# Kernel optimization log

Hardware: AMD Instinct MI355X
Metric: run time of the kernel (lower is better)

## Reference

```python
import jax, jax.numpy as jnp
import numpy as np

B, LQ, H, NH, LK, N = 32, 256, 256, 8, 512, 8192
DH = H // NH
EPS = 1e-12

def layer_norm(x, g, b):
    m = x.mean(-1, keepdims=True)
    v = ((x - m) ** 2).mean(-1, keepdims=True)
    return (x - m) / jnp.sqrt(v + EPS) * g + b

def setup_inputs() -> dict:
    rs = np.random.RandomState(0)
    counts = rs.randint(LK // 2, LK + 1, size=B)  # ragged per-graph edge counts, max = LK
    E = int(counts.sum())
    edge_batch = jnp.asarray(np.repeat(np.arange(B), counts), jnp.int32)
    edge_pos = jnp.asarray(np.concatenate([np.arange(c) for c in counts]), jnp.int32)
    pad_mask = jnp.asarray((np.arange(LK)[None, :] < counts[:, None]).astype(np.float32))
    src = jnp.asarray(rs.randint(0, N, E), jnp.int32)
    dst = jnp.asarray(rs.randint(0, N, E), jnp.int32)
    ks = jax.random.split(jax.random.key(0), 16)
    def rn(i, shape, s=0.02):
        return jax.random.normal(ks[i], shape, jnp.float32) * s
    return dict(
        extended_attention_mask=jnp.zeros((B, 1, 1, LQ), jnp.float32),
        query=rn(0, (B, LQ, H), 1.0),
        rel_embedding_output=rn(1, (E, H), 1.0),
        graph_output=rn(2, (N, H), 1.0),
        src=src, dst=dst, edge_batch=edge_batch, edge_pos=edge_pos, pad_mask=pad_mask,
        Wq=rn(3, (H, H)), bq=jnp.zeros((H,), jnp.float32),
        Wk=rn(4, (2 * H, H)), bk=jnp.zeros((H,), jnp.float32),
        Wv=rn(5, (H, H)), bv=jnp.zeros((H,), jnp.float32),
        Wo=rn(6, (H, H)), bo=jnp.zeros((H,), jnp.float32),
        ln1_g=jnp.ones((H,), jnp.float32), ln1_b=jnp.zeros((H,), jnp.float32),
        W1=rn(7, (H, H)), b1=jnp.zeros((H,), jnp.float32),
        W2=rn(8, (H, H)), b2=jnp.zeros((H,), jnp.float32),
        ln2_g=jnp.ones((H,), jnp.float32), ln2_b=jnp.zeros((H,), jnp.float32),
    )

def reference(extended_attention_mask, query, rel_embedding_output, graph_output,
              src, dst, edge_batch, edge_pos, pad_mask,
              Wq, bq, Wk, bk, Wv, bv, Wo, bo, ln1_g, ln1_b,
              W1, b1, W2, b2, ln2_g, ln2_b):
    # --- memory_transform: edge gather + ragged pad (vectorized scatter) ---
    key_flat = jnp.concatenate([graph_output[src], rel_embedding_output], -1)  # [E, 2H]
    dst_flat = graph_output[dst]                                               # [E, H]
    key_pad = jnp.zeros((B, LK, 2 * H), key_flat.dtype).at[edge_batch, edge_pos].set(key_flat)
    val_pad = jnp.zeros((B, LK, H), dst_flat.dtype).at[edge_batch, edge_pos].set(dst_flat)
    cross_mask = (1.0 - pad_mask)[:, None, None, :] * -10000.0                 # [B,1,1,LK]
    # --- BidiAttention ---
    Q = (query @ Wq + bq).reshape(B, LQ, NH, DH)
    K = (key_pad @ Wk + bk).reshape(B, LK, NH, DH)
    V = (val_pad @ Wv + bv).reshape(B, LK, NH, DH)
    scores = jnp.einsum('bqhd,bkhd->bhqk', Q, K) / np.float32(np.sqrt(DH))
    pq = jax.nn.softmax(scores + cross_mask, axis=-1)
    query_ctx = jnp.einsum('bhqk,bkhd->bqhd', pq, V).reshape(B, LQ, H)
    pv = jax.nn.softmax(scores.transpose(0, 1, 3, 2) + extended_attention_mask, axis=-1)
    value_ctx = jnp.einsum('bhkq,bqhd->bkhd', pv, Q).reshape(B, LK, H)
    # --- RelAwareCross output / gate ---
    query_out = layer_norm(query_ctx @ Wo + bo + query, ln1_g, ln1_b)
    theta = jax.nn.sigmoid(value_ctx @ W1 + b1 + val_pad @ W2 + b2)
    value_new = layer_norm(theta * value_ctx + (1.0 - theta) * val_pad, ln2_g, ln2_b)
    # --- memory_update: unpad + scatter-mean by dst, replace rows with incoming edges ---
    val_edges = value_new[edge_batch, edge_pos]                                # [E, H]
    sums = jax.ops.segment_sum(val_edges, dst, num_segments=N)
    cnts = jax.ops.segment_sum(jnp.ones((val_edges.shape[0],), val_edges.dtype), dst, num_segments=N)
    mean = sums / jnp.maximum(cnts, 1.0)[:, None]
    graph_new = jnp.where((cnts > 0)[:, None], mean, graph_output)
    return (graph_new, query_out)
```

## Files before the change

### kernel.cpp

```cpp
#include <hip/hip_runtime.h>
#include <hip/hip_bf16.h>
#include <string.h>

#define B_ 32
#define LQ_ 256
#define H_ 256
#define NH_ 8
#define LK_ 512
#define N_ 8192
#define DH_ 32

typedef float floatx4 __attribute__((ext_vector_type(4)));
typedef short shortx8 __attribute__((ext_vector_type(8)));

__device__ __forceinline__ short f2b(float f) {
    __hip_bfloat16 h = __float2bfloat16(f);
    short s;
    __builtin_memcpy(&s, &h, 2);
    return s;
}
__device__ __forceinline__ float b2f(short s) {
    unsigned u = ((unsigned)(unsigned short)s) << 16;
    float f;
    __builtin_memcpy(&f, &u, 4);
    return f;
}

__global__ __launch_bounds__(256) void phase1(
    const float* __restrict__ graph, const float* __restrict__ rel,
    const int* __restrict__ src, const int* __restrict__ dst,
    const int* __restrict__ eb, const float* __restrict__ pad_mask,
    const float* __restrict__ Wq, const float* __restrict__ Wk,
    const float* __restrict__ Wv, const float* __restrict__ Wo,
    const float* __restrict__ W1, const float* __restrict__ W2,
    short* __restrict__ WT, short* __restrict__ key_pad,
    short* __restrict__ val_pad, float* __restrict__ zbase, int E) {
    const int bid = blockIdx.x, tid = threadIdx.x;
    if (bid < 8192) {
        int row = bid * 2 + (tid >> 7);
        int t = tid & 127;
        int b = row >> 9, p = row & 511;
        bool valid = pad_mask[row] > 0.5f;
        size_t krow = (size_t)row * 512;
        size_t vrow = (size_t)row * 256;
        int kc = t * 4, vc = t * 2;
        if (valid) {
            int lo = 0, hi = E;
            while (lo < hi) { int mid = (lo + hi) >> 1; if (eb[mid] < b) lo = mid + 1; else hi = mid; }
            int e = lo + p;
            int s = src[e], d = dst[e];
            const float* sp = (kc < 256) ? (graph + (size_t)s * 256 + kc)
                                         : (rel + (size_t)e * 256 + (kc - 256));
            float4 k4 = *(const float4*)sp;
            key_pad[krow + kc + 0] = f2b(k4.x);
            key_pad[krow + kc + 1] = f2b(k4.y);
            key_pad[krow + kc + 2] = f2b(k4.z);
            key_pad[krow + kc + 3] = f2b(k4.w);
            float2 v2 = *(const float2*)(graph + (size_t)d * 256 + vc);
            val_pad[vrow + vc + 0] = f2b(v2.x);
            val_pad[vrow + vc + 1] = f2b(v2.y);
        } else {
            *(long long*)&key_pad[krow + kc] = 0;
            *(int*)&val_pad[vrow + vc] = 0;
        }
    } else if (bid < 9984) {
        int i = (bid - 8192) * 256 + tid;
        const float* s;
        int K, loc;
        if (i < 65536) { s = Wq; K = 256; loc = i; }
        else if (i < 196608) { s = Wk; K = 512; loc = i - 65536; }
        else {
            int m = (i - 196608) >> 16;
            loc = (i - 196608) & 65535;
            K = 256;
            s = (m == 0) ? Wv : (m == 1) ? Wo : (m == 2) ? W1 : W2;
        }
        int n = loc / K, k = loc - n * K;
        WT[i] = f2b(s[(size_t)k * 256 + n]);
    } else {
        long long n = (long long)N_ * H_ + N_;
        for (long long i = (long long)(bid - 9984) * 256 + tid; i < n; i += 512 * 256)
            zbase[i] = 0.f;
    }
}

__global__ __launch_bounds__(256) void phase2_gemm(
    const float* __restrict__ query, const short* __restrict__ key_pad,
    const short* __restrict__ val_pad, const short* __restrict__ WT,
    const float* __restrict__ bq, const float* __restrict__ bk,
    const float* __restrict__ bv,
    short* __restrict__ Qb, short* __restrict__ Kb, short* __restrict__ Vb) {
    __shared__ short As[64][40];
    __shared__ short Bs[64][40];
    const int tid = threadIdx.x;
    const int id = blockIdx.x;
    const float* Af = nullptr;
    const short* Ab = nullptr;
    const short* WTp;
    const float* bias;
    short* C;
    int K, rb, cb;
    if (id < 512) { rb = id >> 2; cb = id & 3; Af = query; K = 256; WTp = WT; bias = bq; C = Qb; }
    else if (id < 1536) { int t = id - 512; rb = t >> 2; cb = t & 3; Ab = key_pad; K = 512; WTp = WT + 65536; bias = bk; C = Kb; }
    else { int t = id - 1536; rb = t >> 2; cb = t & 3; Ab = val_pad; K = 256; WTp = WT + 196608; bias = bv; C = Vb; }
    const int row0 = rb * 64, col0 = cb * 64;
    const int wv = tid >> 6, lane = tid & 63;
    const int mw = (wv & 1) * 32, nw = (wv >> 1) * 32;
    const int lm = lane & 15, quad = lane >> 4;

    floatx4 acc[2][2] = {{{0.f, 0.f, 0.f, 0.f}, {0.f, 0.f, 0.f, 0.f}},
                         {{0.f, 0.f, 0.f, 0.f}, {0.f, 0.f, 0.f, 0.f}}};

    for (int kc = 0; kc < K; kc += 32) {
        {
            int r = tid >> 2, kq = (tid & 3) * 8;
            if (Af) {
                const float* ap = Af + (size_t)(row0 + r) * K + kc + kq;
                float4 a1 = *(const float4*)ap, a2 = *(const float4*)(ap + 4);
                As[r][kq + 0] = f2b(a1.x); As[r][kq + 1] = f2b(a1.y);
                As[r][kq + 2] = f2b(a1.z); As[r][kq + 3] = f2b(a1.w);
                As[r][kq + 4] = f2b(a2.x); As[r][kq + 5] = f2b(a2.y);
                As[r][kq + 6] = f2b(a2.z); As[r][kq + 7] = f2b(a2.w);
            } else {
                *(shortx8*)&As[r][kq] =
                    *(const shortx8*)(Ab + (size_t)(row0 + r) * K + kc + kq);
            }
        }
        {
            int n = tid >> 2, kq = (tid & 3) * 8;
            *(shortx8*)&Bs[n][kq] =
                *(const shortx8*)(WTp + (size_t)(col0 + n) * K + kc + kq);
        }
        __syncthreads();
        shortx8 a0 = *(const shortx8*)&As[mw + lm][quad * 8];
        shortx8 a1 = *(const shortx8*)&As[mw + 16 + lm][quad * 8];
        shortx8 b0 = *(const shortx8*)&Bs[nw + lm][quad * 8];
        shortx8 b1 = *(const shortx8*)&Bs[nw + 16 + lm][quad * 8];
        acc[0][0] = __builtin_amdgcn_mfma_f32_16x16x32_bf16(a0, b0, acc[0][0], 0, 0, 0);
        acc[0][1] = __builtin_amdgcn_mfma_f32_16x16x32_bf16(a0, b1, acc[0][1], 0, 0, 0);
        acc[1][0] = __builtin_amdgcn_mfma_f32_16x16x32_bf16(a1, b0, acc[1][0], 0, 0, 0);
        acc[1][1] = __builtin_amdgcn_mfma_f32_16x16x32_bf16(a1, b1, acc[1][1], 0, 0, 0);
        __syncthreads();
    }
#pragma unroll
    for (int i = 0; i < 2; i++) {
#pragma unroll
        for (int j = 0; j < 2; j++) {
            int gn = col0 + nw + j * 16 + lm;
            float bvv = bias[gn];
#pragma unroll
            for (int r = 0; r < 4; r++) {
                int gm = row0 + mw + i * 16 + quad * 4 + r;
                C[(size_t)gm * 256 + gn] = f2b(acc[i][j][r] + bvv);
            }
        }
    }
}

__global__ __launch_bounds__(256) void phase3_attn(
    const short* __restrict__ Qm, const short* __restrict__ Km,
    const short* __restrict__ Vm, const float* __restrict__ pad_mask,
    const float* __restrict__ ext, short* __restrict__ qctx,
    short* __restrict__ vctx) {
    __shared__ short SB1[64][40];
    __shared__ short SB2[128][40];
    __shared__ short SB3[32][136];
    __shared__ short SB4[64][136];
    __shared__ float rowinv[64];
    const int tid = threadIdx.x;
    const int wv = tid >> 6, lane = tid & 63;
    const int lm = lane & 15, quad = lane >> 4;
    const float scale = 0.17677669529663687f;
    const int id = blockIdx.x;

    if (id < 1024) {
        const int q0 = (id & 3) * 64, h = (id >> 2) & 7, b = id >> 5;
        {
            int r = tid >> 2, dq = (tid & 3) * 8;
            *(shortx8*)&SB1[r][dq] =
                *(const shortx8*)(Qm + ((size_t)(b * LQ_ + q0 + r)) * H_ + h * DH_ + dq);
        }
        floatx4 oacc0 = {0.f, 0.f, 0.f, 0.f}, oacc1 = {0.f, 0.f, 0.f, 0.f};
        float psum[4] = {0.f, 0.f, 0.f, 0.f};
        shortx8 aq;
        for (int c = 0; c < 4; c++) {
            const int kbase = c * 128;
            {
                int r = tid >> 1, dq = (tid & 1) * 16;
                const short* kp = Km + ((size_t)(b * LK_ + kbase + r)) * H_ + h * DH_ + dq;
                *(shortx8*)&SB2[r][dq] = *(const shortx8*)kp;
                *(shortx8*)&SB2[r][dq + 8] = *(const shortx8*)(kp + 8);
                const short* vp = Vm + ((size_t)(b * LK_ + kbase + r)) * H_ + h * DH_ + dq;
                shortx8 v1 = *(const shortx8*)vp;
                shortx8 v2 = *(const shortx8*)(vp + 8);
#pragma unroll
                for (int i = 0; i < 8; i++) {
                    SB3[dq + i][r] = v1[i];
                    SB3[dq + 8 + i][r] = v2[i];
                }
            }
            __syncthreads();
            if (c == 0) aq = *(const shortx8*)&SB1[wv * 16 + lm][quad * 8];
#pragma unroll
            for (int nt = 0; nt < 8; nt++) {
                shortx8 bk = *(const shortx8*)&SB2[nt * 16 + lm][quad * 8];
                floatx4 s = {0.f, 0.f, 0.f, 0.f};
                s = __builtin_amdgcn_mfma_f32_16x16x32_bf16(aq, bk, s, 0, 0, 0);
                float mk = (1.0f - pad_mask[b * LK_ + kbase + nt * 16 + lm]) * -10000.0f;
#pragma unroll
                for (int r = 0; r < 4; r++) {
                    float e = __expf(s[r] * scale + mk);
                    psum[r] += e;
                    SB4[wv * 16 + quad * 4 + r][nt * 16 + lm] = f2b(e);
                }
            }
            __syncthreads();
#pragma unroll
            for (int kk = 0; kk < 4; kk++) {
                shortx8 pa = *(const shortx8*)&SB4[wv * 16 + lm][kk * 32 + quad * 8];
                shortx8 b0 = *(const shortx8*)&SB3[lm][kk * 32 + quad * 8];
                shortx8 b1 = *(const shortx8*)&SB3[16 + lm][kk * 32 + quad * 8];
                oacc0 = __builtin_amdgcn_mfma_f32_16x16x32_bf16(pa, b0, oacc0, 0, 0, 0);
                oacc1 = __builtin_amdgcn_mfma_f32_16x16x32_bf16(pa, b1, oacc1, 0, 0, 0);
            }
            __syncthreads();
        }
#pragma unroll
        for (int r = 0; r < 4; r++) {
            float s2 = psum[r];
            s2 += __shfl_down(s2, 8, 64);
            s2 += __shfl_down(s2, 4, 64);
            s2 += __shfl_down(s2, 2, 64);
            s2 += __shfl_down(s2, 1, 64);
            if (lm == 0) rowinv[wv * 16 + quad * 4 + r] = 1.0f / s2;
        }
        __syncthreads();
#pragma unroll
        for (int r = 0; r < 4; r++) {
            float inv = rowinv[wv * 16 + quad * 4 + r];
            int q = q0 + wv * 16 + quad * 4 + r;
            short* op = qctx + ((size_t)(b * LQ_ + q)) * H_ + h * DH_;
            op[lm] = f2b(oacc0[r] * inv);
            op[16 + lm] = f2b(oacc1[r] * inv);
        }
    } else {
        const int id2 = id - 1024;
        const int k0 = (id2 & 7) * 64, h = (id2 >> 3) & 7, b = id2 >> 6;
        {
            int r = tid >> 2, dq = (tid & 3) * 8;
            *(shortx8*)&SB1[r][dq] =
                *(const shortx8*)(Km + ((size_t)(b * LK_ + k0 + r)) * H_ + h * DH_ + dq);
        }
        floatx4 oacc0 = {0.f, 0.f, 0.f, 0.f}, oacc1 = {0.f, 0.f, 0.f, 0.f};
        float psum[4] = {0.f, 0.f, 0.f, 0.f};
        shortx8 ak;
        for (int c = 0; c < 2; c++) {
            const int qbase = c * 128;
            {
                int r = tid >> 1, dq = (tid & 1) * 16;
                const short* qp = Qm + ((size_t)(b * LQ_ + qbase + r)) * H_ + h * DH_ + dq;
                shortx8 q1 = *(const shortx8*)qp;
                shortx8 q2 = *(const shortx8*)(qp + 8);
                *(shortx8*)&SB2[r][dq] = q1;
                *(shortx8*)&SB2[r][dq + 8] = q2;
#pragma unroll
                for (int i = 0; i < 8; i++) {
                    SB3[dq + i][r] = q1[i];
                    SB3[dq + 8 + i][r] = q2[i];
                }
            }
            __syncthreads();
            if (c == 0) ak = *(const shortx8*)&SB1[wv * 16 + lm][quad * 8];
#pragma unroll
            for (int nt = 0; nt < 8; nt++) {
                shortx8 bq = *(const shortx8*)&SB2[nt * 16 + lm][quad * 8];
                floatx4 s = {0.f, 0.f, 0.f, 0.f};
                s = __builtin_amdgcn_mfma_f32_16x16x32_bf16(ak, bq, s, 0, 0, 0);
                float mk = ext[b * LQ_ + qbase + nt * 16 + lm];
#pragma unroll
                for (int r = 0; r < 4; r++) {
                    float e = __expf(s[r] * scale + mk);
                    psum[r] += e;
                    SB4[wv * 16 + quad * 4 + r][nt * 16 + lm] = f2b(e);
                }
            }
            __syncthreads();
#pragma unroll
            for (int kk = 0; kk < 4; kk++) {
                shortx8 pa = *(const shortx8*)&SB4[wv * 16 + lm][kk * 32 + quad * 8];
                shortx8 b0 = *(const shortx8*)&SB3[lm][kk * 32 + quad * 8];
                shortx8 b1 = *(const shortx8*)&SB3[16 + lm][kk * 32 + quad * 8];
                oacc0 = __builtin_amdgcn_mfma_f32_16x16x32_bf16(pa, b0, oacc0, 0, 0, 0);
                oacc1 = __builtin_amdgcn_mfma_f32_16x16x32_bf16(pa, b1, oacc1, 0, 0, 0);
            }
            __syncthreads();
        }
#pragma unroll
        for (int r = 0; r < 4; r++) {
            float s2 = psum[r];
            s2 += __shfl_down(s2, 8, 64);
            s2 += __shfl_down(s2, 4, 64);
            s2 += __shfl_down(s2, 2, 64);
            s2 += __shfl_down(s2, 1, 64);
            if (lm == 0) rowinv[wv * 16 + quad * 4 + r] = 1.0f / s2;
        }
        __syncthreads();
#pragma unroll
        for (int r = 0; r < 4; r++) {
            float inv = rowinv[wv * 16 + quad * 4 + r];
            int k = k0 + wv * 16 + quad * 4 + r;
            short* op = vctx + ((size_t)(b * LK_ + k)) * H_ + h * DH_;
            op[lm] = f2b(oacc0[r] * inv);
            op[16 + lm] = f2b(oacc1[r] * inv);
        }
    }
}

__global__ __launch_bounds__(256) void phase4a_gemm(
    const short* __restrict__ qctx, const short* __restrict__ vctx,
    const short* __restrict__ val_pad, const short* __restrict__ WTo,
    const short* __restrict__ WT1, const short* __restrict__ WT2,
    float* __restrict__ obuf, float* __restrict__ tbuf) {
    __shared__ short As1[64][40];
    __shared__ short As2[64][40];
    __shared__ short Bs1[64][40];
    __shared__ short Bs2[64][40];
    const int tid = threadIdx.x;
    const int id = blockIdx.x;
    const bool is_out = id < 512;
    int t = is_out ? id : id - 512;
    const int row0 = (t >> 2) * 64, col0 = (t & 3) * 64;
    const int wv = tid >> 6, lane = tid & 63;
    const int mw = (wv & 1) * 32, nw = (wv >> 1) * 32;
    const int lm = lane & 15, quad = lane >> 4;

    floatx4 acc[2][2] = {{{0.f, 0.f, 0.f, 0.f}, {0.f, 0.f, 0.f, 0.f}},
                         {{0.f, 0.f, 0.f, 0.f}, {0.f, 0.f, 0.f, 0.f}}};

    for (int kc = 0; kc < 256; kc += 32) {
        int r = tid >> 2, kq = (tid & 3) * 8;
        if (is_out) {
            *(shortx8*)&As1[r][kq] =
                *(const shortx8*)(qctx + (size_t)(row0 + r) * 256 + kc + kq);
            *(shortx8*)&Bs1[r][kq] =
                *(const shortx8*)(WTo + (size_t)(col0 + r) * 256 + kc + kq);
        } else {
            *(shortx8*)&As1[r][kq] =
                *(const shortx8*)(vctx + (size_t)(row0 + r) * 256 + kc + kq);
            *(shortx8*)&As2[r][kq] =
                *(const shortx8*)(val_pad + (size_t)(row0 + r) * 256 + kc + kq);
            *(shortx8*)&Bs1[r][kq] =
                *(const shortx8*)(WT1 + (size_t)(col0 + r) * 256 + kc + kq);
            *(shortx8*)&Bs2[r][kq] =
                *(const shortx8*)(WT2 + (size_t)(col0 + r) * 256 + kc + kq);
        }
        __syncthreads();
        shortx8 a0 = *(const shortx8*)&As1[mw + lm][quad * 8];
        shortx8 a1 = *(const shortx8*)&As1[mw + 16 + lm][quad * 8];
        shortx8 b0 = *(const shortx8*)&Bs1[nw + lm][quad * 8];
        shortx8 b1 = *(const shortx8*)&Bs1[nw + 16 + lm][quad * 8];
        acc[0][0] = __builtin_amdgcn_mfma_f32_16x16x32_bf16(a0, b0, acc[0][0], 0, 0, 0);
        acc[0][1] = __builtin_amdgcn_mfma_f32_16x16x32_bf16(a0, b1, acc[0][1], 0, 0, 0);
        acc[1][0] = __builtin_amdgcn_mfma_f32_16x16x32_bf16(a1, b0, acc[1][0], 0, 0, 0);
        acc[1][1] = __builtin_amdgcn_mfma_f32_16x16x32_bf16(a1, b1, acc[1][1], 0, 0, 0);
        if (!is_out) {
            shortx8 c0 = *(const shortx8*)&As2[mw + lm][quad * 8];
            shortx8 c1 = *(const shortx8*)&As2[mw + 16 + lm][quad * 8];
            shortx8 d0 = *(const shortx8*)&Bs2[nw + lm][quad * 8];
            shortx8 d1 = *(const shortx8*)&Bs2[nw + 16 + lm][quad * 8];
            acc[0][0] = __builtin_amdgcn_mfma_f32_16x16x32_bf16(c0, d0, acc[0][0], 0, 0, 0);
            acc[0][1] = __builtin_amdgcn_mfma_f32_16x16x32_bf16(c0, d1, acc[0][1], 0, 0, 0);
            acc[1][0] = __builtin_amdgcn_mfma_f32_16x16x32_bf16(c1, d0, acc[1][0], 0, 0, 0);
            acc[1][1] = __builtin_amdgcn_mfma_f32_16x16x32_bf16(c1, d1, acc[1][1], 0, 0, 0);
        }
        __syncthreads();
    }
    float* C = is_out ? obuf : tbuf;
#pragma unroll
    for (int i = 0; i < 2; i++) {
#pragma unroll
        for (int j = 0; j < 2; j++) {
            int gn = col0 + nw + j * 16 + lm;
#pragma unroll
            for (int r = 0; r < 4; r++) {
                int gm = row0 + mw + i * 16 + quad * 4 + r;
                C[(size_t)gm * 256 + gn] = acc[i][j][r];
            }
        }
    }
}

__global__ __launch_bounds__(256) void phase4b_ln(
    const float* __restrict__ obuf, const float* __restrict__ bo,
    const float* __restrict__ query, const float* __restrict__ g1,
    const float* __restrict__ be1, float* __restrict__ out_q,
    const float* __restrict__ tbuf, const short* __restrict__ vctx,
    const short* __restrict__ val_pad, const float* __restrict__ b1_,
    const float* __restrict__ b2_, const float* __restrict__ g2,
    const float* __restrict__ be2, const float* __restrict__ pad_mask,
    const int* __restrict__ eb, const int* __restrict__ dst,
    float* __restrict__ sums, int* __restrict__ icnts, int E) {
    __shared__ float red[8];
    const int c = threadIdx.x;
    const int wave = c >> 6;
    if (blockIdx.x < 8192) {
        int row = blockIdx.x;
        long long idx = (long long)row * H_ + c;
        float x = obuf[idx] + bo[c] + query[idx];
        float t = x;
        for (int off = 32; off > 0; off >>= 1) t += __shfl_down(t, off, 64);
        if ((c & 63) == 0) red[wave] = t;
        __syncthreads();
        float mean = (red[0] + red[1] + red[2] + red[3]) * (1.0f / H_);
        float dv = x - mean;
        float v = dv * dv;
        for (int off = 32; off > 0; off >>= 1) v += __shfl_down(v, off, 64);
        if ((c & 63) == 0) red[4 + wave] = v;
        __syncthreads();
        float var = (red[4] + red[5] + red[6] + red[7]) * (1.0f / H_);
        out_q[idx] = dv * rsqrtf(var + 1e-12f) * g1[c] + be1[c];
    } else {
        int row = blockIdx.x - 8192;
        bool valid = pad_mask[row] > 0.5f;
        if (!valid) return;
        long long idx = (long long)row * H_ + c;
        float th = 1.0f / (1.0f + __expf(-(tbuf[idx] + b1_[c] + b2_[c])));
        float x = th * b2f(vctx[idx]) + (1.0f - th) * b2f(val_pad[idx]);
        float t = x;
        for (int off = 32; off > 0; off >>= 1) t += __shfl_down(t, off, 64);
        if ((c & 63) == 0) red[wave] = t;
        __syncthreads();
        float mean = (red[0] + red[1] + red[2] + red[3]) * (1.0f / H_);
        float dv = x - mean;
        float v = dv * dv;
        for (int off = 32; off > 0; off >>= 1) v += __shfl_down(v, off, 64);
        if ((c & 63) == 0) red[4 + wave] = v;
        __syncthreads();
        float var = (red[4] + red[5] + red[6] + red[7]) * (1.0f / H_);
        float y = dv * rsqrtf(var + 1e-12f) * g2[c] + be2[c];
        int b = row >> 9;
        int lo = 0, hi = E;
        while (lo < hi) { int mid = (lo + hi) >> 1; if (eb[mid] < b) lo = mid + 1; else hi = mid; }
        int d = dst[lo + (row & 511)];
        atomicAdd(&sums[(size_t)d * 256 + c], y);
        if (c == 0) atomicAdd(&icnts[d], 1);
    }
}

__global__ __launch_bounds__(256) void finalize_graph(
    const float* __restrict__ sums, const int* __restrict__ icnts,
    const float* __restrict__ graph, float* __restrict__ out_g) {
    int n = blockIdx.x, c = threadIdx.x;
    long long idx = (long long)n * H_ + c;
    int cnt = icnts[n];
    out_g[idx] = (cnt > 0) ? sums[idx] / (float)cnt : graph[idx];
}

extern "C" void kernel_launch(void* const* d_in, const int* in_sizes, int n_in,
                              void* d_out, int out_size, void* d_ws, size_t ws_size,
                              hipStream_t stream) {
    const float* ext_mask = (const float*)d_in[0];
    const float* query    = (const float*)d_in[1];
    const float* rel      = (const float*)d_in[2];
    const float* graph    = (const float*)d_in[3];
    const int*  src      = (const int*)d_in[4];
    const int*  dst      = (const int*)d_in[5];
    const int*  eb       = (const int*)d_in[6];
    const int*  ep       = (const int*)d_in[7];
    const float* pad_mask = (const float*)d_in[8];
    const float* Wq = (const float*)d_in[9];  const float* bq = (const float*)d_in[10];
    const float* Wk = (const float*)d_in[11]; const float* bk = (const float*)d_in[12];
    const float* Wv = (const float*)d_in[13]; const float* bv = (const float*)d_in[14];
    const float* Wo = (const float*)d_in[15]; const float* bo = (const float*)d_in[16];
    const float* g1 = (const float*)d_in[17]; const float* be1 = (const float*)d_in[18];
    const float* W1 = (const float*)d_in[19]; const float* b1 = (const float*)d_in[20];
    const float* W2 = (const float*)d_in[21]; const float* b2 = (const float*)d_in[22];
    const float* g2 = (const float*)d_in[23]; const float* be2 = (const float*)d_in[24];
    const int E = in_sizes[2] / H_;

    float* out_g = (float*)d_out;
    float* out_q = (float*)d_out + (size_t)N_ * H_;

    short* sp = (short*)d_ws;
    short* key_pad = sp; sp += (size_t)B_ * LK_ * 2 * H_;
    short* val_pad = sp; sp += (size_t)B_ * LK_ * H_;
    short* Qb      = sp; sp += (size_t)B_ * LQ_ * H_;
    short* Kb      = sp; sp += (size_t)B_ * LK_ * H_;
    short* Vb      = sp; sp += (size_t)B_ * LK_ * H_;
    short* qctx    = sp; sp += (size_t)B_ * LQ_ * H_;
    short* vctx    = sp; sp += (size_t)B_ * LK_ * H_;
    short* WT      = sp; sp += 458752;
    short* WTo = WT + 262144;
    short* WT1 = WT + 327680;
    short* WT2 = WT + 393216;
    float* fp = (float*)(((size_t)sp + 15) & ~(size_t)15);
    float* sums = fp; fp += (size_t)N_ * H_;
    int*   icnts = (int*)fp; fp += N_;
    float* obuf = fp; fp += (size_t)B_ * LQ_ * H_;
    float* tbuf = fp; fp += (size_t)B_ * LK_ * H_;

    phase1<<<10496, 256, 0, stream>>>(graph, rel, src, dst, eb, pad_mask,
                                      Wq, Wk, Wv, Wo, W1, W2,
                                      WT, key_pad, val_pad, sums, E);
    phase2_gemm<<<2560, 256, 0, stream>>>(query, key_pad, val_pad, WT,
                                          bq, bk, bv, Qb, Kb, Vb);
    phase3_attn<<<3072, 256, 0, stream>>>(Qb, Kb, Vb, pad_mask, ext_mask,
                                          qctx, vctx);
    phase4a_gemm<<<1536, 256, 0, stream>>>(qctx, vctx, val_pad, WTo, WT1, WT2,
                                           obuf, tbuf);
    phase4b_ln<<<24576, 256, 0, stream>>>(obuf, bo, query, g1, be1, out_q,
                                          tbuf, vctx, val_pad, b1, b2, g2, be2,
                                          pad_mask, eb, dst, sums, icnts, E);
    finalize_graph<<<N_, 256, 0, stream>>>(sums, icnts, graph, out_g);
}
```

Baseline: 273.1 us.

## Emit transposed V and Q from projection GEMM and restructure attention MFMA operand order

The projection GEMM now writes V and an extra copy of Q in transposed (head-dim-major) layout by swapping the A/B operands, so the attention kernel can load them with vector copies instead of scalar LDS transposes. The attention kernel swaps operand order so each lane owns a full softmax row. This removes the shared-memory row-sum reduction and one barrier per chunk, and lets outputs be stored as vector writes. It also switches to exp2 with the scale folded in, and adds a launch-bounds occupancy hint. In exchange the GEMM runs 512 extra blocks and writes an extra Q copy.

Result: slower. 291.8 us (+6.9%).

```diff
diff --git a/kernel.cpp b/kernel.cpp
--- a/kernel.cpp
+++ b/kernel.cpp
@@ -12,6 +12,7 @@
 
 typedef float floatx4 __attribute__((ext_vector_type(4)));
 typedef short shortx8 __attribute__((ext_vector_type(8)));
+typedef short shortx4 __attribute__((ext_vector_type(4)));
 
 __device__ __forceinline__ short f2b(float f) {
     __hip_bfloat16 h = __float2bfloat16(f);
@@ -25,6 +26,8 @@
     __builtin_memcpy(&f, &u, 4);
     return f;
 }
+
+#define LOG2E 1.44269504088896f
 
 __global__ __launch_bounds__(256) void phase1(
     const float* __restrict__ graph, const float* __restrict__ rel,
@@ -89,21 +92,41 @@
     const short* __restrict__ val_pad, const short* __restrict__ WT,
     const float* __restrict__ bq, const float* __restrict__ bk,
     const float* __restrict__ bv,
-    short* __restrict__ Qb, short* __restrict__ Kb, short* __restrict__ Vb) {
+    short* __restrict__ Qb, short* __restrict__ Kb,
+    short* __restrict__ Vt, short* __restrict__ Qt) {
     __shared__ short As[64][40];
     __shared__ short Bs[64][40];
     const int tid = threadIdx.x;
     const int id = blockIdx.x;
-    const float* Af = nullptr;
-    const short* Ab = nullptr;
-    const short* WTp;
-    const float* bias;
-    short* C;
-    int K, rb, cb;
-    if (id < 512) { rb = id >> 2; cb = id & 3; Af = query; K = 256; WTp = WT; bias = bq; C = Qb; }
-    else if (id < 1536) { int t = id - 512; rb = t >> 2; cb = t & 3; Ab = key_pad; K = 512; WTp = WT + 65536; bias = bk; C = Kb; }
-    else { int t = id - 1536; rb = t >> 2; cb = t & 3; Ab = val_pad; K = 256; WTp = WT + 196608; bias = bv; C = Vb; }
-    const int row0 = rb * 64, col0 = cb * 64;
+    const float* Af = nullptr; const short* Ab = nullptr;
+    const float* Bf = nullptr; const short* Bb = nullptr;
+    const float* bias; short* C;
+    size_t cbase; int cstride, K; bool biasM;
+    if (id < 512) {
+        int rb = id >> 2, cb = id & 3;
+        Af = query + (size_t)(rb * 64) * 256; K = 256;
+        Bb = WT + (size_t)(cb * 64) * 256;
+        bias = bq + cb * 64; biasM = false;
+        C = Qb; cbase = (size_t)(rb * 64) * 256 + cb * 64; cstride = 256;
+    } else if (id < 1536) {
+        int t = id - 512; int rb = t >> 2, cb = t & 3;
+        Ab = key_pad + (size_t)(rb * 64) * 512; K = 512;
+        Bb = WT + 65536 + (size_t)(cb * 64) * 512;
+        bias = bk + cb * 64; biasM = false;
+        C = Kb; cbase = (size_t)(rb * 64) * 256 + cb * 64; cstride = 256;
+    } else if (id < 2560) {
+        int t = id - 1536; int b = t >> 5, ct = (t >> 3) & 3, kt = t & 7;
+        Ab = WT + 196608 + (size_t)(ct * 64) * 256; K = 256;
+        Bb = val_pad + ((size_t)(b * 512 + kt * 64)) * 256;
+        bias = bv + ct * 64; biasM = true;
+        C = Vt; cbase = ((size_t)(b * 256 + ct * 64)) * 512 + kt * 64; cstride = 512;
+    } else {
+        int t = id - 2560; int b = t >> 4, ct = (t >> 2) & 3, qt = t & 3;
+        Ab = WT + (size_t)(ct * 64) * 256; K = 256;
+        Bf = query + ((size_t)(b * 256 + qt * 64)) * 256;
+        bias = bq + ct * 64; biasM = true;
+        C = Qt; cbase = ((size_t)(b * 256 + ct * 64)) * 256 + qt * 64; cstride = 256;
+    }
     const int wv = tid >> 6, lane = tid & 63;
     const int mw = (wv & 1) * 32, nw = (wv >> 1) * 32;
     const int lm = lane & 15, quad = lane >> 4;
@@ -112,24 +135,26 @@
                          {{0.f, 0.f, 0.f, 0.f}, {0.f, 0.f, 0.f, 0.f}}};
 
     for (int kc = 0; kc < K; kc += 32) {
-        {
-            int r = tid >> 2, kq = (tid & 3) * 8;
-            if (Af) {
-                const float* ap = Af + (size_t)(row0 + r) * K + kc + kq;
-                float4 a1 = *(const float4*)ap, a2 = *(const float4*)(ap + 4);
-                As[r][kq + 0] = f2b(a1.x); As[r][kq + 1] = f2b(a1.y);
-                As[r][kq + 2] = f2b(a1.z); As[r][kq + 3] = f2b(a1.w);
-                As[r][kq + 4] = f2b(a2.x); As[r][kq + 5] = f2b(a2.y);
-                As[r][kq + 6] = f2b(a2.z); As[r][kq + 7] = f2b(a2.w);
-            } else {
-                *(shortx8*)&As[r][kq] =
-                    *(const shortx8*)(Ab + (size_t)(row0 + r) * K + kc + kq);
-            }
-        }
-        {
-            int n = tid >> 2, kq = (tid & 3) * 8;
-            *(shortx8*)&Bs[n][kq] =
-                *(const shortx8*)(WTp + (size_t)(col0 + n) * K + kc + kq);
+        int r = tid >> 2, kq = (tid & 3) * 8;
+        if (Af) {
+            const float* ap = Af + (size_t)r * K + kc + kq;
+            float4 a1 = *(const float4*)ap, a2 = *(const float4*)(ap + 4);
+            As[r][kq + 0] = f2b(a1.x); As[r][kq + 1] = f2b(a1.y);
+            As[r][kq + 2] = f2b(a1.z); As[r][kq + 3] = f2b(a1.w);
+            As[r][kq + 4] = f2b(a2.x); As[r][kq + 5] = f2b(a2.y);
+            As[r][kq + 6] = f2b(a2.z); As[r][kq + 7] = f2b(a2.w);
+        } else {
+            *(shortx8*)&As[r][kq] = *(const shortx8*)(Ab + (size_t)r * K + kc + kq);
+        }
+        if (Bf) {
+            const float* bp = Bf + (size_t)r * K + kc + kq;
+            float4 b1 = *(const float4*)bp, b2 = *(const float4*)(bp + 4);
+            Bs[r][kq + 0] = f2b(b1.x); Bs[r][kq + 1] = f2b(b1.y);
+            Bs[r][kq + 2] = f2b(b1.z); Bs[r][kq + 3] = f2b(b1.w);
+            Bs[r][kq + 4] = f2b(b2.x); Bs[r][kq + 5] = f2b(b2.y);
+            Bs[r][kq + 6] = f2b(b2.z); Bs[r][kq + 7] = f2b(b2.w);
+        } else {
+            *(shortx8*)&Bs[r][kq] = *(const shortx8*)(Bb + (size_t)r * K + kc + kq);
         }
         __syncthreads();
         shortx8 a0 = *(const shortx8*)&As[mw + lm][quad * 8];
@@ -146,173 +171,153 @@
     for (int i = 0; i < 2; i++) {
 #pragma unroll
         for (int j = 0; j < 2; j++) {
-            int gn = col0 + nw + j * 16 + lm;
-            float bvv = bias[gn];
+            int gn = nw + j * 16 + lm;
 #pragma unroll
             for (int r = 0; r < 4; r++) {
-                int gm = row0 + mw + i * 16 + quad * 4 + r;
-                C[(size_t)gm * 256 + gn] = f2b(acc[i][j][r] + bvv);
-            }
-        }
-    }
-}
-
-__global__ __launch_bounds__(256) void phase3_attn(
+                int gm = mw + i * 16 + quad * 4 + r;
+                float bvv = biasM ? bias[gm] : bias[gn];
+                C[cbase + (size_t)gm * cstride + gn] = f2b(acc[i][j][r] + bvv);
+            }
+        }
+    }
+}
+
+__global__ __launch_bounds__(256, 4) void phase3_attn(
     const short* __restrict__ Qm, const short* __restrict__ Km,
-    const short* __restrict__ Vm, const float* __restrict__ pad_mask,
-    const float* __restrict__ ext, short* __restrict__ qctx,
-    short* __restrict__ vctx) {
-    __shared__ short SB1[64][40];
+    const short* __restrict__ Vt, const short* __restrict__ Qt,
+    const float* __restrict__ pad_mask, const float* __restrict__ ext,
+    short* __restrict__ qctx, short* __restrict__ vctx) {
     __shared__ short SB2[128][40];
     __shared__ short SB3[32][136];
     __shared__ short SB4[64][136];
-    __shared__ float rowinv[64];
     const int tid = threadIdx.x;
     const int wv = tid >> 6, lane = tid & 63;
     const int lm = lane & 15, quad = lane >> 4;
-    const float scale = 0.17677669529663687f;
+    const float scale2 = 0.17677669529663687f * LOG2E;
     const int id = blockIdx.x;
 
     if (id < 1024) {
         const int q0 = (id & 3) * 64, h = (id >> 2) & 7, b = id >> 5;
-        {
-            int r = tid >> 2, dq = (tid & 3) * 8;
-            *(shortx8*)&SB1[r][dq] =
-                *(const shortx8*)(Qm + ((size_t)(b * LQ_ + q0 + r)) * H_ + h * DH_ + dq);
-        }
+        shortx8 bqf = *(const shortx8*)(
+            Qm + ((size_t)(b * 256 + q0 + wv * 16 + lm)) * 256 + h * 32 + quad * 8);
         floatx4 oacc0 = {0.f, 0.f, 0.f, 0.f}, oacc1 = {0.f, 0.f, 0.f, 0.f};
-        float psum[4] = {0.f, 0.f, 0.f, 0.f};
-        shortx8 aq;
+        float psum = 0.f;
         for (int c = 0; c < 4; c++) {
             const int kbase = c * 128;
             {
                 int r = tid >> 1, dq = (tid & 1) * 16;
-                const short* kp = Km + ((size_t)(b * LK_ + kbase + r)) * H_ + h * DH_ + dq;
+                const short* kp = Km + ((size_t)(b * 512 + kbase + r)) * 256 + h * 32 + dq;
                 *(shortx8*)&SB2[r][dq] = *(const shortx8*)kp;
                 *(shortx8*)&SB2[r][dq + 8] = *(const shortx8*)(kp + 8);
-                const short* vp = Vm + ((size_t)(b * LK_ + kbase + r)) * H_ + h * DH_ + dq;
-                shortx8 v1 = *(const shortx8*)vp;
-                shortx8 v2 = *(const shortx8*)(vp + 8);
-#pragma unroll
-                for (int i = 0; i < 8; i++) {
-                    SB3[dq + i][r] = v1[i];
-                    SB3[dq + 8 + i][r] = v2[i];
+            }
+            {
+                int r = tid >> 3, kq = (tid & 7) * 16;
+                const short* vp = Vt + ((size_t)(b * 256 + h * 32 + r)) * 512 + kbase + kq;
+                *(shortx8*)&SB3[r][kq] = *(const shortx8*)vp;
+                *(shortx8*)&SB3[r][kq + 8] = *(const shortx8*)(vp + 8);
+            }
+            __syncthreads();
+            const floatx4* pmp = (const floatx4*)(pad_mask + b * 512 + kbase);
+#pragma unroll
+            for (int nt = 0; nt < 8; nt++) {
+                shortx8 ak = *(const shortx8*)&SB2[nt * 16 + lm][quad * 8];
+                floatx4 s = {0.f, 0.f, 0.f, 0.f};
+                s = __builtin_amdgcn_mfma_f32_16x16x32_bf16(ak, bqf, s, 0, 0, 0);
+                floatx4 pm = pmp[nt * 4 + quad];
+                shortx4 p4;
+#pragma unroll
+                for (int r = 0; r < 4; r++) {
+                    float e = __builtin_amdgcn_exp2f(
+                        s[r] * scale2 + (1.0f - pm[r]) * (-10000.0f * LOG2E));
+                    psum += e;
+                    p4[r] = f2b(e);
                 }
+                *(long long*)&SB4[wv * 16 + lm][nt * 16 + quad * 4] = *(long long*)&p4;
+            }
+#pragma unroll
+            for (int kk = 0; kk < 4; kk++) {
+                shortx8 pb = *(const shortx8*)&SB4[wv * 16 + lm][kk * 32 + quad * 8];
+                shortx8 a0 = *(const shortx8*)&SB3[lm][kk * 32 + quad * 8];
+                shortx8 a1 = *(const shortx8*)&SB3[16 + lm][kk * 32 + quad * 8];
+                oacc0 = __builtin_amdgcn_mfma_f32_16x16x32_bf16(a0, pb, oacc0, 0, 0, 0);
+                oacc1 = __builtin_amdgcn_mfma_f32_16x16x32_bf16(a1, pb, oacc1, 0, 0, 0);
             }
             __syncthreads();
-            if (c == 0) aq = *(const shortx8*)&SB1[wv * 16 + lm][quad * 8];
-#pragma unroll
-            for (int nt = 0; nt < 8; nt++) {
-                shortx8 bk = *(const shortx8*)&SB2[nt * 16 + lm][quad * 8];
-                floatx4 s = {0.f, 0.f, 0.f, 0.f};
-                s = __builtin_amdgcn_mfma_f32_16x16x32_bf16(aq, bk, s, 0, 0, 0);
-                float mk = (1.0f - pad_mask[b * LK_ + kbase + nt * 16 + lm]) * -10000.0f;
-#pragma unroll
-                for (int r = 0; r < 4; r++) {
-                    float e = __expf(s[r] * scale + mk);
-                    psum[r] += e;
-                    SB4[wv * 16 + quad * 4 + r][nt * 16 + lm] = f2b(e);
-                }
-            }
-            __syncthreads();
-#pragma unroll
-            for (int kk = 0; kk < 4; kk++) {
-                shortx8 pa = *(const shortx8*)&SB4[wv * 16 + lm][kk * 32 + quad * 8];
-                shortx8 b0 = *(const shortx8*)&SB3[lm][kk * 32 + quad * 8];
-                shortx8 b1 = *(const shortx8*)&SB3[16 + lm][kk * 32 + quad * 8];
-                oacc0 = __builtin_amdgcn_mfma_f32_16x16x32_bf16(pa, b0, oacc0, 0, 0, 0);
-                oacc1 = __builtin_amdgcn_mfma_f32_16x16x32_bf16(pa, b1, oacc1, 0, 0, 0);
-            }
-            __syncthreads();
-        }
+        }
+        psum += __shfl_xor(psum, 16, 64);
+        psum += __shfl_xor(psum, 32, 64);
+        float inv = 1.0f / psum;
+        int q = q0 + wv * 16 + lm;
+        short* op = qctx + ((size_t)(b * 256 + q)) * 256 + h * 32;
+        shortx4 o0, o1;
 #pragma unroll
         for (int r = 0; r < 4; r++) {
-            float s2 = psum[r];
-            s2 += __shfl_down(s2, 8, 64);
-            s2 += __shfl_down(s2, 4, 64);
-            s2 += __shfl_down(s2, 2, 64);
-            s2 += __shfl_down(s2, 1, 64);
-            if (lm == 0) rowinv[wv * 16 + quad * 4 + r] = 1.0f / s2;
-        }
-        __syncthreads();
-#pragma unroll
-        for (int r = 0; r < 4; r++) {
-            float inv = rowinv[wv * 16 + quad * 4 + r];
-            int q = q0 + wv * 16 + quad * 4 + r;
-            short* op = qctx + ((size_t)(b * LQ_ + q)) * H_ + h * DH_;
-            op[lm] = f2b(oacc0[r] * inv);
-            op[16 + lm] = f2b(oacc1[r] * inv);
-        }
+            o0[r] = f2b(oacc0[r] * inv);
+            o1[r] = f2b(oacc1[r] * inv);
+        }
+        *(long long*)(op + quad * 4) = *(long long*)&o0;
+        *(long long*)(op + 16 + quad * 4) = *(long long*)&o1;
     } else {
         const int id2 = id - 1024;
         const int k0 = (id2 & 7) * 64, h = (id2 >> 3) & 7, b = id2 >> 6;
-        {
-            int r = tid >> 2, dq = (tid & 3) * 8;
-            *(shortx8*)&SB1[r][dq] =
-                *(const shortx8*)(Km + ((size_t)(b * LK_ + k0 + r)) * H_ + h * DH_ + dq);
-        }
+        shortx8 bkf = *(const shortx8*)(
+            Km + ((size_t)(b * 512 + k0 + wv * 16 + lm)) * 256 + h * 32 + quad * 8);
         floatx4 oacc0 = {0.f, 0.f, 0.f, 0.f}, oacc1 = {0.f, 0.f, 0.f, 0.f};
-        float psum[4] = {0.f, 0.f, 0.f, 0.f};
-        shortx8 ak;
+        float psum = 0.f;
         for (int c = 0; c < 2; c++) {
             const int qbase = c * 128;
             {
                 int r = tid >> 1, dq = (tid & 1) * 16;
-                const short* qp = Qm + ((size_t)(b * LQ_ + qbase + r)) * H_ + h * DH_ + dq;
-                shortx8 q1 = *(const shortx8*)qp;
-                shortx8 q2 = *(const shortx8*)(qp + 8);
-                *(shortx8*)&SB2[r][dq] = q1;
-                *(shortx8*)&SB2[r][dq + 8] = q2;
-#pragma unroll
-                for (int i = 0; i < 8; i++) {
-                    SB3[dq + i][r] = q1[i];
-                    SB3[dq + 8 + i][r] = q2[i];
+                const short* qp = Qm + ((size_t)(b * 256 + qbase + r)) * 256 + h * 32 + dq;
+                *(shortx8*)&SB2[r][dq] = *(const shortx8*)qp;
+                *(shortx8*)&SB2[r][dq + 8] = *(const shortx8*)(qp + 8);
+            }
+            {
+                int r = tid >> 3, kq = (tid & 7) * 16;
+                const short* tp = Qt + ((size_t)(b * 256 + h * 32 + r)) * 256 + qbase + kq;
+                *(shortx8*)&SB3[r][kq] = *(const shortx8*)tp;
+                *(shortx8*)&SB3[r][kq + 8] = *(const shortx8*)(tp + 8);
+            }
+            __syncthreads();
+            const floatx4* emp = (const floatx4*)(ext + b * 256 + qbase);
+#pragma unroll
+            for (int nt = 0; nt < 8; nt++) {
+                shortx8 aq = *(const shortx8*)&SB2[nt * 16 + lm][quad * 8];
+                floatx4 s = {0.f, 0.f, 0.f, 0.f};
+                s = __builtin_amdgcn_mfma_f32_16x16x32_bf16(aq, bkf, s, 0, 0, 0);
+                floatx4 em = emp[nt * 4 + quad];
+                shortx4 p4;
+#pragma unroll
+                for (int r = 0; r < 4; r++) {
+                    float e = __builtin_amdgcn_exp2f(s[r] * scale2 + em[r] * LOG2E);
+                    psum += e;
+                    p4[r] = f2b(e);
                 }
+                *(long long*)&SB4[wv * 16 + lm][nt * 16 + quad * 4] = *(long long*)&p4;
+            }
+#pragma unroll
+            for (int kk = 0; kk < 4; kk++) {
+                shortx8 pb = *(const shortx8*)&SB4[wv * 16 + lm][kk * 32 + quad * 8];
+                shortx8 a0 = *(const shortx8*)&SB3[lm][kk * 32 + quad * 8];
+                shortx8 a1 = *(const shortx8*)&SB3[16 + lm][kk * 32 + quad * 8];
+                oacc0 = __builtin_amdgcn_mfma_f32_16x16x32_bf16(a0, pb, oacc0, 0, 0, 0);
+                oacc1 = __builtin_amdgcn_mfma_f32_16x16x32_bf16(a1, pb, oacc1, 0, 0, 0);
             }
             __syncthreads();
-            if (c == 0) ak = *(const shortx8*)&SB1[wv * 16 + lm][quad * 8];
-#pragma unroll
-            for (int nt = 0; nt < 8; nt++) {
-                shortx8 bq = *(const shortx8*)&SB2[nt * 16 + lm][quad * 8];
-                floatx4 s = {0.f, 0.f, 0.f, 0.f};
-                s = __builtin_amdgcn_mfma_f32_16x16x32_bf16(ak, bq, s, 0, 0, 0);
-                float mk = ext[b * LQ_ + qbase + nt * 16 + lm];
-#pragma unroll
-                for (int r = 0; r < 4; r++) {
-                    float e = __expf(s[r] * scale + mk);
-                    psum[r] += e;
-                    SB4[wv * 16 + quad * 4 + r][nt * 16 + lm] = f2b(e);
-                }
-            }
-            __syncthreads();
-#pragma unroll
-            for (int kk = 0; kk < 4; kk++) {
-                shortx8 pa = *(const shortx8*)&SB4[wv * 16 + lm][kk * 32 + quad * 8];
-                shortx8 b0 = *(const shortx8*)&SB3[lm][kk * 32 + quad * 8];
-                shortx8 b1 = *(const shortx8*)&SB3[16 + lm][kk * 32 + quad * 8];
-                oacc0 = __builtin_amdgcn_mfma_f32_16x16x32_bf16(pa, b0, oacc0, 0, 0, 0);
-                oacc1 = __builtin_amdgcn_mfma_f32_16x16x32_bf16(pa, b1, oacc1, 0, 0, 0);
-            }
-            __syncthreads();
-        }
+        }
+        psum += __shfl_xor(psum, 16, 64);
+        psum += __shfl_xor(psum, 32, 64);
+        float inv = 1.0f / psum;
+        int k = k0 + wv * 16 + lm;
+        short* op = vctx + ((size_t)(b * 512 + k)) * 256 + h * 32;
+        shortx4 o0, o1;
 #pragma unroll
         for (int r = 0; r < 4; r++) {
-            float s2 = psum[r];
-            s2 += __shfl_down(s2, 8, 64);
-            s2 += __shfl_down(s2, 4, 64);
-            s2 += __shfl_down(s2, 2, 64);
-            s2 += __shfl_down(s2, 1, 64);
-            if (lm == 0) rowinv[wv * 16 + quad * 4 + r] = 1.0f / s2;
-        }
-        __syncthreads();
-#pragma unroll
-        for (int r = 0; r < 4; r++) {
-            float inv = rowinv[wv * 16 + quad * 4 + r];
-            int k = k0 + wv * 16 + quad * 4 + r;
-            short* op = vctx + ((size_t)(b * LK_ + k)) * H_ + h * DH_;
-            op[lm] = f2b(oacc0[r] * inv);
-            op[16 + lm] = f2b(oacc1[r] * inv);
-        }
+            o0[r] = f2b(oacc0[r] * inv);
+            o1[r] = f2b(oacc1[r] * inv);
+        }
+        *(long long*)(op + quad * 4) = *(long long*)&o0;
+        *(long long*)(op + 16 + quad * 4) = *(long long*)&o1;
     }
 }
 
@@ -477,6 +482,7 @@
     const float* W2 = (const float*)d_in[21]; const float* b2 = (const float*)d_in[22];
     const float* g2 = (const float*)d_in[23]; const float* be2 = (const float*)d_in[24];
     const int E = in_sizes[2] / H_;
+    (void)ep;
 
     float* out_g = (float*)d_out;
     float* out_q = (float*)d_out + (size_t)N_ * H_;
@@ -486,7 +492,8 @@
     short* val_pad = sp; sp += (size_t)B_ * LK_ * H_;
     short* Qb      = sp; sp += (size_t)B_ * LQ_ * H_;
     short* Kb      = sp; sp += (size_t)B_ * LK_ * H_;
-    short* Vb      = sp; sp += (size_t)B_ * LK_ * H_;
+    short* Vt      = sp; sp += (size_t)B_ * H_ * LK_;
+    short* Qt      = sp; sp += (size_t)B_ * H_ * LQ_;
     short* qctx    = sp; sp += (size_t)B_ * LQ_ * H_;
     short* vctx    = sp; sp += (size_t)B_ * LK_ * H_;
     short* WT      = sp; sp += 458752;
@@ -502,9 +509,9 @@
     phase1<<<10496, 256, 0, stream>>>(graph, rel, src, dst, eb, pad_mask,
                                       Wq, Wk, Wv, Wo, W1, W2,
                                       WT, key_pad, val_pad, sums, E);
-    phase2_gemm<<<2560, 256, 0, stream>>>(query, key_pad, val_pad, WT,
-                                          bq, bk, bv, Qb, Kb, Vb);
-    phase3_attn<<<3072, 256, 0, stream>>>(Qb, Kb, Vb, pad_mask, ext_mask,
+    phase2_gemm<<<3072, 256, 0, stream>>>(query, key_pad, val_pad, WT,
+                                          bq, bk, bv, Qb, Kb, Vt, Qt);
+    phase3_attn<<<3072, 256, 0, stream>>>(Qb, Kb, Vt, Qt, pad_mask, ext_mask,
                                           qctx, vctx);
     phase4a_gemm<<<1536, 256, 0, stream>>>(qctx, vctx, val_pad, WTo, WT1, WT2,
                                            obuf, tbuf);
```
